# Performance work log

Measured on AMD Instinct MI355X. Metric: run time of the kernel, lower is better.

Reference implementation:

```python
import jax, jax.numpy as jnp
import numpy as np

B, N, IN_DIM, L_DIM, H_DIM, N_CLASSES, FLOW_LEN = 128, 512, 128, 64, 64, 10, 4


def setup_inputs() -> dict:
    key = jax.random.key(0)
    ks = jax.random.split(key, 20)
    s = 0.05
    return {
        "gs": jax.random.uniform(ks[0], (B, N, N), dtype=jnp.float32),
        "hs": jax.random.normal(ks[1], (B, N, IN_DIM), dtype=jnp.float32),
        "labels": jax.random.randint(ks[2], (B,), 0, N_CLASSES),
        "eps": jax.random.normal(ks[3], (B, N, 1), dtype=jnp.float32),
        "W_s": jax.random.normal(ks[4], (IN_DIM, L_DIM), dtype=jnp.float32) * s,
        "b_s": jnp.zeros((L_DIM,), jnp.float32),
        "W_mu": jax.random.normal(ks[5], (L_DIM, 1), dtype=jnp.float32) * s,
        "b_mu": jnp.zeros((1,), jnp.float32),
        "W_lv": jax.random.normal(ks[6], (L_DIM, 1), dtype=jnp.float32) * s,
        "b_lv": jnp.zeros((1,), jnp.float32),
        "W_dec": jax.random.normal(ks[7], (1, L_DIM), dtype=jnp.float32) * s,
        "b_dec": jnp.zeros((L_DIM,), jnp.float32),
        "W1": jax.random.normal(ks[8], (L_DIM, H_DIM), dtype=jnp.float32) * s,
        "b1": jnp.zeros((H_DIM,), jnp.float32),
        "W2": jax.random.normal(ks[9], (H_DIM, N_CLASSES), dtype=jnp.float32) * s,
        "b2": jnp.zeros((N_CLASSES,), jnp.float32),
        "beta": jax.random.uniform(ks[10], (1,), jnp.float32, 0.0, 100.0),
        "fw": jax.random.normal(ks[11], (FLOW_LEN,), dtype=jnp.float32) * 0.1,
        "fb": jax.random.normal(ks[12], (FLOW_LEN,), dtype=jnp.float32) * 0.1,
        "fs": jax.random.normal(ks[13], (FLOW_LEN,), dtype=jnp.float32) * 0.1,
    }


def reference(gs, hs, labels, eps, W_s, b_s, W_mu, b_mu, W_lv, b_lv,
              W_dec, b_dec, W1, b1, W2, b2, beta, fw, fb, fs):
    relu = jax.nn.relu
    # norm_g: g / g.sum(1) (torch broadcast divides column j by row-sum deg[j])
    deg = gs.sum(axis=2)                       # [B, N]
    g = gs / deg[:, None, :]                   # [B, N, N]

    def gcn(g, h, W, b):
        return relu(jnp.einsum('bij,bjf->bif', g, h) @ W + b)

    h = gcn(g, hs, W_s, b_s)                   # [B, N, L]
    r = h
    mu = gcn(g, h, W_mu, b_mu)                 # [B, N, 1]
    logvar = gcn(g, h, W_lv, b_lv)             # [B, N, 1]
    sigma = jnp.exp(0.5 * logvar)
    z0 = eps * sigma + mu                      # reparameterize (training)

    # 4-step planar flow on scalar latent; log-det accumulated on pre-transform z
    z = z0
    log_jac = jnp.zeros_like(z0)
    for k in range(FLOW_LEN):
        t = jnp.tanh(fw[k] * z + fb[k])
        det = 1.0 + fs[k] * fw[k] * (1.0 - t * t)
        log_jac = log_jac + jnp.log(jnp.abs(det) + 1e-7)
        z = z + fs[k] * t
    zk = z

    # KL = log q(z0) - log_jac - log p(zk), loggaussian = -0.5*((z-mu)/s)^2 - log(2.5 s)
    logq = -0.5 * ((z0 - mu) / sigma) ** 2 - jnp.log(2.5 * sigma)
    logp = -0.5 * zk ** 2 - jnp.log(jnp.float32(2.5))
    kl = logq - log_jac - logp                 # [B, N, 1]

    zs = jax.nn.sigmoid(beta * zk)             # [B, N, 1]
    d = gcn(g, zs, W_dec, b_dec)               # [B, N, L]
    hg = jnp.einsum('bnl,bn->bl', h, zs[..., 0])  # h.T @ zk, [B, L]

    # classify
    x = relu(hg @ W1 + b1)
    logits = jax.nn.log_softmax(x @ W2 + b2, axis=1)  # [B, C]

    nll = -jnp.mean(logits[jnp.arange(B), labels])
    mse = jnp.mean((r - d) ** 2)
    loss = nll + mse + kl.mean()
    preds = jnp.argmax(logits, axis=1)
    acc = jnp.mean((preds == labels).astype(jnp.float32))
    return jnp.stack([loss, acc])
```

## Files before the change

kernel.cpp:

```cpp
#include <hip/hip_runtime.h>
#include <hip/hip_bf16.h>

#define BB 128
#define NN 512
#define IND 128
#define LD 64
#define NC 10
#define FL 4
#define ROWS (BB*NN)
#define HALF 256
#define QTR 128

#define OFF_ACC 0
#define OFF_RDEG (OFF_ACC + 8)
#define OFF_VM   (OFF_RDEG + ROWS)
#define OFF_VV   (OFF_VM + ROWS)
#define OFF_ZS   (OFF_VV + ROWS)
#define OFF_ZSS  (OFF_ZS + ROWS)
#define OFF_KLP  (OFF_ZSS + ROWS)
#define OFF_MSEP (OFF_KLP + 512)
#define OFF_XHG  (OFF_MSEP + 512)
#define OFF_H    (OFF_XHG + BB*256)
#define OFF_GSB  (OFF_H + ROWS*32)
#define WS_NEED ((size_t)(OFF_GSB + (size_t)ROWS*256) * 4)

typedef __attribute__((ext_vector_type(8))) short short8v;
typedef __attribute__((ext_vector_type(4))) float f32x4;

__device__ inline float wave_reduce(float v) {
    #pragma unroll
    for (int m = 32; m; m >>= 1) v += __shfl_xor(v, m, 64);
    return v;
}

__device__ inline short f2bf(float f) {
    unsigned u = __float_as_uint(f);
    u += 0x7fff + ((u >> 16) & 1);
    return (short)(u >> 16);
}

__device__ inline float bf2f(short s) {
    return __uint_as_float(((unsigned)(unsigned short)s) << 16);
}

__global__ __launch_bounds__(256) void k_deg(const float* __restrict__ gs,
                                             float* __restrict__ rdeg,
                                             float* __restrict__ accums,
                                             unsigned short* __restrict__ gsb) {
    if (blockIdx.x == 0 && threadIdx.x < 8) accums[threadIdx.x] = 0.f;
    int t = threadIdx.x;
    int row = blockIdx.x * 4 + (t >> 6), lane = t & 63;
    const float4* r4 = (const float4*)(gs + (size_t)row * NN) + lane * 2;
    float4 a = r4[0], b = r4[1];
    float s = a.x + a.y + a.z + a.w + b.x + b.y + b.z + b.w;
    float sr = wave_reduce(s);
    if (lane == 0) rdeg[row] = 1.0f / sr;
    if (gsb) {
        short8v v;
        v[0] = f2bf(a.x); v[1] = f2bf(a.y); v[2] = f2bf(a.z); v[3] = f2bf(a.w);
        v[4] = f2bf(b.x); v[5] = f2bf(b.y); v[6] = f2bf(b.z); v[7] = f2bf(b.w);
        *(short8v*)(gsb + (size_t)row * NN + lane * 8) = v;
    }
}

template<bool BF>
__global__ __launch_bounds__(1024) void k_hwgemm(
    const float* __restrict__ gs, const unsigned short* __restrict__ gsb,
    const float* __restrict__ hs, const float* __restrict__ W_s,
    const float* __restrict__ b_s, const float* __restrict__ W_mu,
    const float* __restrict__ W_lv, const float* __restrict__ rdeg_ws,
    unsigned short* __restrict__ h_ws, float* __restrict__ vm_ws,
    float* __restrict__ vv_ws)
{
    __shared__ unsigned short s_hwT[64 * 512];
    __shared__ unsigned short s_h[HALF * 64];
    __shared__ float s_rdeg[NN];

    const int tid = threadIdx.x, lane = tid & 63, wid = tid >> 6;
    const int b = blockIdx.x >> 1, p = blockIdx.x & 1, rbase = p * HALF;

    if (tid < NN) s_rdeg[tid] = rdeg_ws[(size_t)b * NN + tid];

    unsigned short* sWT = s_h;
    {
        const float4* wp = (const float4*)W_s + tid * 2;
        float4 w0 = wp[0], w1 = wp[1];
        int k = tid >> 3, l0 = (tid & 7) * 8;
        float wv[8] = {w0.x, w0.y, w0.z, w0.w, w1.x, w1.y, w1.z, w1.w};
        #pragma unroll
        for (int e = 0; e < 8; ++e) {
            int l = l0 + e;
            int byte = (l * 256 + k * 2) ^ ((l & 7) << 4);
            *(unsigned short*)((char*)sWT + byte) = (unsigned short)f2bf(wv[e]);
        }
    }
    __syncthreads();

    {
        int n0 = wid * 32, cq = lane & 15, koq = lane >> 4;
        f32x4 accB[2][4] = {};
        #pragma unroll
        for (int kk = 0; kk < 4; ++kk) {
            short8v bf[4];
            #pragma unroll
            for (int lt = 0; lt < 4; ++lt) {
                int l = lt * 16 + cq;
                int byte = (l * 256 + (kk * 32 + koq * 8) * 2) ^ ((l & 7) << 4);
                bf[lt] = *(const short8v*)((char*)sWT + byte);
            }
            #pragma unroll
            for (int nt = 0; nt < 2; ++nt) {
                int row = n0 + nt * 16 + cq;
                const float4* hp = (const float4*)(hs + ((size_t)b * NN + row) * IND
                                                   + kk * 32 + koq * 8);
                float4 h0 = hp[0], h1 = hp[1];
                short8v a;
                a[0] = f2bf(h0.x); a[1] = f2bf(h0.y); a[2] = f2bf(h0.z); a[3] = f2bf(h0.w);
                a[4] = f2bf(h1.x); a[5] = f2bf(h1.y); a[6] = f2bf(h1.z); a[7] = f2bf(h1.w);
                #pragma unroll
                for (int lt = 0; lt < 4; ++lt)
                    accB[nt][lt] = __builtin_amdgcn_mfma_f32_16x16x32_bf16(a, bf[lt], accB[nt][lt], 0, 0, 0);
            }
        }
        __syncthreads();
        int r0 = (lane >> 4) * 4;
        #pragma unroll
        for (int nt = 0; nt < 2; ++nt)
            #pragma unroll
            for (int lt = 0; lt < 4; ++lt)
                #pragma unroll
                for (int q = 0; q < 4; ++q) {
                    int n = n0 + nt * 16 + r0 + q;
                    int l = lt * 16 + cq;
                    int byte = (l * 1024 + n * 2) ^ ((l & 7) << 4);
                    *(unsigned short*)((char*)s_hwT + byte) =
                        (unsigned short)f2bf(accB[nt][lt][q] * s_rdeg[n]);
                }
    }
    __syncthreads();

    {
        int cq = lane & 15, koq = lane >> 4;
        int rowl = wid * 16 + cq, rowg = rbase + rowl;
        const unsigned short* A16 = gsb + ((size_t)b * NN + rowg) * NN + koq * 8;
        const float* A32 = gs + ((size_t)b * NN + rowg) * NN + koq * 8;
        f32x4 accC[4] = {};
        for (int kk = 0; kk < 16; ++kk) {
            short8v bf[4];
            #pragma unroll
            for (int lt = 0; lt < 4; ++lt) {
                int l = lt * 16 + cq;
                int byte = (l * 1024 + (kk * 32 + koq * 8) * 2) ^ ((l & 7) << 4);
                bf[lt] = *(const short8v*)((char*)s_hwT + byte);
            }
            short8v a;
            if constexpr (BF) {
                a = *(const short8v*)(A16 + kk * 32);
            } else {
                const float4* gp = (const float4*)(A32 + kk * 32);
                float4 g0 = gp[0], g1 = gp[1];
                a[0] = f2bf(g0.x); a[1] = f2bf(g0.y); a[2] = f2bf(g0.z); a[3] = f2bf(g0.w);
                a[4] = f2bf(g1.x); a[5] = f2bf(g1.y); a[6] = f2bf(g1.z); a[7] = f2bf(g1.w);
            }
            #pragma unroll
            for (int lt = 0; lt < 4; ++lt)
                accC[lt] = __builtin_amdgcn_mfma_f32_16x16x32_bf16(a, bf[lt], accC[lt], 0, 0, 0);
        }
        int r0 = (lane >> 4) * 4;
        float bsv[4];
        #pragma unroll
        for (int lt = 0; lt < 4; ++lt) bsv[lt] = b_s[lt * 16 + cq];
        #pragma unroll
        for (int lt = 0; lt < 4; ++lt)
            #pragma unroll
            for (int q = 0; q < 4; ++q) {
                int nloc = wid * 16 + r0 + q;
                int l = lt * 16 + cq;
                s_h[nloc * 64 + l] = (unsigned short)f2bf(fmaxf(accC[lt][q] + bsv[lt], 0.f));
            }
    }
    __syncthreads();

    {
        int rowl = tid >> 2, off = (tid & 3) * 16;
        unsigned short* dst = h_ws + ((size_t)(b * NN + rbase + rowl)) * 64 + off;
        const unsigned short* src = &s_h[rowl * 64 + off];
        *(short8v*)dst = *(const short8v*)src;
        *(short8v*)(dst + 8) = *(const short8v*)(src + 8);
    }

    {
        int g16 = tid >> 4, l16 = tid & 15;
        float wmu[4], wlv[4];
        #pragma unroll
        for (int e = 0; e < 4; ++e) { wmu[e] = W_mu[l16 * 4 + e]; wlv[e] = W_lv[l16 * 4 + e]; }
        #pragma unroll
        for (int rr = 0; rr < 4; ++rr) {
            int rowl = g16 * 4 + rr;
            const unsigned short* hp = &s_h[rowl * 64 + l16 * 4];
            float pm = 0.f, pv = 0.f;
            #pragma unroll
            for (int e = 0; e < 4; ++e) {
                float hv = bf2f((short)hp[e]);
                pm += hv * wmu[e]; pv += hv * wlv[e];
            }
            #pragma unroll
            for (int m = 1; m <= 8; m <<= 1) {
                pm += __shfl_xor(pm, m, 64);
                pv += __shfl_xor(pv, m, 64);
            }
            if (l16 == 0) {
                float rd = s_rdeg[rbase + rowl];
                vm_ws[(size_t)b * NN + rbase + rowl] = pm * rd;
                vv_ws[(size_t)b * NN + rbase + rowl] = pv * rd;
            }
        }
    }
}

template<bool BF>
__global__ __launch_bounds__(512) void k_muflow(
    const float* __restrict__ gs, const unsigned short* __restrict__ gsb,
    const float* __restrict__ vm_ws, const float* __restrict__ vv_ws,
    const float* __restrict__ eps, const float* __restrict__ b_mu,
    const float* __restrict__ b_lv, const float* __restrict__ beta,
    const float* __restrict__ fw, const float* __restrict__ fb,
    const float* __restrict__ fs, const float* __restrict__ rdeg_ws,
    float* __restrict__ zs_ws, float* __restrict__ zss_ws,
    float* __restrict__ klp)
{
    __shared__ unsigned short s_bmu[NN], s_blv[NN];
    __shared__ float s_mp[QTR], s_lp[QTR];
    __shared__ float s_fin[8];
    const int tid = threadIdx.x, lane = tid & 63, wid = tid >> 6;
    const int b = blockIdx.x >> 2, qb = blockIdx.x & 3, rbase = qb * QTR;

    if (tid < NN) {
        s_bmu[tid] = (unsigned short)f2bf(vm_ws[(size_t)b * NN + tid]);
        s_blv[tid] = (unsigned short)f2bf(vv_ws[(size_t)b * NN + tid]);
    }
    __syncthreads();

    const int cq = lane & 15, koq = lane >> 4;
    const int rowl = wid * 16 + cq, rowg = rbase + rowl;
    const unsigned short* A16 = gsb + ((size_t)b * NN + rowg) * NN + koq * 8;
    const float* A32 = gs + ((size_t)b * NN + rowg) * NN + koq * 8;
    const char* bptr = (cq == 1) ? (const char*)s_blv : (const char*)s_bmu;
    f32x4 acc = {0.f, 0.f, 0.f, 0.f};
    const short8v bz = {0, 0, 0, 0, 0, 0, 0, 0};
    #pragma unroll 4
    for (int kk = 0; kk < 16; ++kk) {
        short8v a;
        if constexpr (BF) {
            a = *(const short8v*)(A16 + kk * 32);
        } else {
            const float4* gp = (const float4*)(A32 + kk * 32);
            float4 g0 = gp[0], g1 = gp[1];
            a[0] = f2bf(g0.x); a[1] = f2bf(g0.y); a[2] = f2bf(g0.z); a[3] = f2bf(g0.w);
            a[4] = f2bf(g1.x); a[5] = f2bf(g1.y); a[6] = f2bf(g1.z); a[7] = f2bf(g1.w);
        }
        short8v bl = *(const short8v*)(bptr + (kk * 32 + koq * 8) * 2);
        short8v bfrag = (cq < 2) ? bl : bz;
        acc = __builtin_amdgcn_mfma_f32_16x16x32_bf16(a, bfrag, acc, 0, 0, 0);
    }
    int r0 = (lane >> 4) * 4;
    if (cq == 0) {
        #pragma unroll
        for (int q2 = 0; q2 < 4; ++q2) s_mp[wid * 16 + r0 + q2] = acc[q2];
    } else if (cq == 1) {
        #pragma unroll
        for (int q2 = 0; q2 < 4; ++q2) s_lp[wid * 16 + r0 + q2] = acc[q2];
    }
    __syncthreads();

    float my_kl = 0.f;
    if (tid < QTR) {
        int rg = rbase + tid;
        float mu = fmaxf(s_mp[tid] + b_mu[0], 0.f);
        float lv = fmaxf(s_lp[tid] + b_lv[0], 0.f);
        float sigma = expf(0.5f * lv);
        float z0 = eps[(size_t)b * NN + rg] * sigma + mu;
        float z = z0, lj = 0.f;
        #pragma unroll
        for (int k = 0; k < FL; ++k) {
            float tt = tanhf(fw[k] * z + fb[k]);
            float det = 1.f + fs[k] * fw[k] * (1.f - tt * tt);
            lj += logf(fabsf(det) + 1e-7f);
            z += fs[k] * tt;
        }
        float e0 = (z0 - mu) / sigma;
        float logq = -0.5f * e0 * e0 - logf(2.5f * sigma);
        float logp = -0.5f * z * z - logf(2.5f);
        my_kl = logq - lj - logp;
        float zv = 1.f / (1.f + expf(-beta[0] * z));
        float rd = rdeg_ws[(size_t)b * NN + rg];
        zs_ws[(size_t)b * NN + rg] = zv;
        zss_ws[(size_t)b * NN + rg] = zv * rd;
    }
    float kv = wave_reduce(my_kl);
    if (lane == 0) s_fin[wid] = kv;
    __syncthreads();
    if (tid == 0) {
        float ks = 0.f;
        #pragma unroll
        for (int w = 0; w < 8; ++w) ks += s_fin[w];
        klp[blockIdx.x] = ks;
    }
}

template<bool BF>
__global__ __launch_bounds__(512) void k_dec(
    const float* __restrict__ gs, const unsigned short* __restrict__ gsb,
    const float* __restrict__ zss_ws, const float* __restrict__ zs_ws,
    const unsigned short* __restrict__ h_ws, const float* __restrict__ W_dec,
    const float* __restrict__ b_dec, float* __restrict__ msep,
    float* __restrict__ xhg)
{
    __shared__ unsigned short s_bz[NN];
    __shared__ float s_zs[QTR];
    __shared__ float s_dp[QTR];
    __shared__ float s_red[8 * 68];
    __shared__ float s_fin[8];
    const int tid = threadIdx.x, lane = tid & 63, wid = tid >> 6;
    const int b = blockIdx.x >> 2, qb = blockIdx.x & 3, rbase = qb * QTR;

    if (tid < NN) s_bz[tid] = (unsigned short)f2bf(zss_ws[(size_t)b * NN + tid]);
    if (tid < QTR) s_zs[tid] = zs_ws[(size_t)b * NN + rbase + tid];
    __syncthreads();

    const int cq = lane & 15, koq = lane >> 4;
    const int rowl = wid * 16 + cq, rowg = rbase + rowl;
    const unsigned short* A16 = gsb + ((size_t)b * NN + rowg) * NN + koq * 8;
    const float* A32 = gs + ((size_t)b * NN + rowg) * NN + koq * 8;
    f32x4 acc = {0.f, 0.f, 0.f, 0.f};
    const short8v bz = {0, 0, 0, 0, 0, 0, 0, 0};
    #pragma unroll 4
    for (int kk = 0; kk < 16; ++kk) {
        short8v a;
        if constexpr (BF) {
            a = *(const short8v*)(A16 + kk * 32);
        } else {
            const float4* gp = (const float4*)(A32 + kk * 32);
            float4 g0 = gp[0], g1 = gp[1];
            a[0] = f2bf(g0.x); a[1] = f2bf(g0.y); a[2] = f2bf(g0.z); a[3] = f2bf(g0.w);
            a[4] = f2bf(g1.x); a[5] = f2bf(g1.y); a[6] = f2bf(g1.z); a[7] = f2bf(g1.w);
        }
        short8v bl = *(const short8v*)((const char*)s_bz + (kk * 32 + koq * 8) * 2);
        short8v bfrag = (cq == 0) ? bl : bz;
        acc = __builtin_amdgcn_mfma_f32_16x16x32_bf16(a, bfrag, acc, 0, 0, 0);
    }
    int r0 = (lane >> 4) * 4;
    if (cq == 0) {
        #pragma unroll
        for (int q2 = 0; q2 < 4; ++q2) s_dp[wid * 16 + r0 + q2] = acc[q2];
    }
    __syncthreads();

    float wd = W_dec[lane], bd = b_dec[lane];
    float msacc = 0.f, hgacc = 0.f;
    #pragma unroll 4
    for (int r = 0; r < 16; ++r) {
        int rl = wid * 16 + r, rg = rbase + rl;
        float dval = fmaxf(s_dp[rl] * wd + bd, 0.f);
        float hval = bf2f((short)h_ws[((size_t)b * NN + rg) * 64 + lane]);
        float diff = hval - dval;
        msacc += diff * diff;
        hgacc += hval * s_zs[rl];
    }
    s_red[wid * 68 + lane] = hgacc;
    float mv = wave_reduce(msacc);
    if (lane == 0) s_fin[wid] = mv;
    __syncthreads();
    if (tid == 0) {
        float ms = 0.f;
        #pragma unroll
        for (int w = 0; w < 8; ++w) ms += s_fin[w];
        msep[blockIdx.x] = ms;
    }
    if (wid == 0) {
        float hgv = 0.f;
        #pragma unroll
        for (int w = 0; w < 8; ++w) hgv += s_red[w * 68 + lane];
        xhg[(size_t)b * 256 + qb * 64 + lane] = hgv;
    }
}

__global__ __launch_bounds__(64) void k_cls(const float* __restrict__ xhg,
                                            const float* __restrict__ klp,
                                            const float* __restrict__ msep,
                                            const float* __restrict__ W1,
                                            const float* __restrict__ b1,
                                            const float* __restrict__ W2,
                                            const float* __restrict__ b2,
                                            const int* __restrict__ labels,
                                            float* __restrict__ accums,
                                            float* __restrict__ out)
{
    __shared__ float s_hg[64], s_x[64], s_lg[12];
    int b = blockIdx.x, l = threadIdx.x;
    s_hg[l] = xhg[(size_t)b * 256 + l] + xhg[(size_t)b * 256 + 64 + l]
            + xhg[(size_t)b * 256 + 128 + l] + xhg[(size_t)b * 256 + 192 + l];
    if (l == 0) atomicAdd(&accums[0], klp[4*b] + klp[4*b+1] + klp[4*b+2] + klp[4*b+3]);
    if (l == 1) atomicAdd(&accums[1], msep[4*b] + msep[4*b+1] + msep[4*b+2] + msep[4*b+3]);
    __syncthreads();
    float x = b1[l];
    #pragma unroll 8
    for (int k = 0; k < LD; ++k) x += s_hg[k] * W1[k * LD + l];
    s_x[l] = fmaxf(x, 0.f);
    __syncthreads();
    if (l < NC) {
        float lg = b2[l];
        #pragma unroll 8
        for (int k = 0; k < LD; ++k) lg += s_x[k] * W2[k * NC + l];
        s_lg[l] = lg;
    }
    __syncthreads();
    if (l == 0) {
        float mx = s_lg[0]; int pred = 0;
        #pragma unroll
        for (int c = 1; c < NC; ++c) if (s_lg[c] > mx) { mx = s_lg[c]; pred = c; }
        float se = 0.f;
        #pragma unroll
        for (int c = 0; c < NC; ++c) se += expf(s_lg[c] - mx);
        int lab = labels[b];
        atomicAdd(&accums[2], -(s_lg[lab] - (mx + logf(se))));
        if (pred == lab) atomicAdd(&accums[3], 1.0f);
        __threadfence();
        unsigned old = atomicAdd((unsigned*)&accums[4], 1u);
        if (old == BB - 1) {
            float kk = atomicAdd(&accums[0], 0.f);
            float mm = atomicAdd(&accums[1], 0.f);
            float nn = atomicAdd(&accums[2], 0.f);
            float aa = atomicAdd(&accums[3], 0.f);
            out[0] = nn / (float)BB
                   + mm / ((float)BB * NN * LD)
                   + kk / ((float)BB * NN);
            out[1] = aa / (float)BB;
        }
    }
}

extern "C" void kernel_launch(void* const* d_in, const int* in_sizes, int n_in,
                              void* d_out, int out_size, void* d_ws, size_t ws_size,
                              hipStream_t stream) {
    const float* gs    = (const float*)d_in[0];
    const float* hs    = (const float*)d_in[1];
    const int*   labels= (const int*)d_in[2];
    const float* eps   = (const float*)d_in[3];
    const float* W_s   = (const float*)d_in[4];
    const float* b_s   = (const float*)d_in[5];
    const float* W_mu  = (const float*)d_in[6];
    const float* b_mu  = (const float*)d_in[7];
    const float* W_lv  = (const float*)d_in[8];
    const float* b_lv  = (const float*)d_in[9];
    const float* W_dec = (const float*)d_in[10];
    const float* b_dec = (const float*)d_in[11];
    const float* W1    = (const float*)d_in[12];
    const float* b1    = (const float*)d_in[13];
    const float* W2    = (const float*)d_in[14];
    const float* b2    = (const float*)d_in[15];
    const float* beta  = (const float*)d_in[16];
    const float* fw    = (const float*)d_in[17];
    const float* fb    = (const float*)d_in[18];
    const float* fs    = (const float*)d_in[19];

    float* ws      = (float*)d_ws;
    float* accums  = ws + OFF_ACC;
    float* rdeg    = ws + OFF_RDEG;
    float* vm_ws   = ws + OFF_VM;
    float* vv_ws   = ws + OFF_VV;
    float* zs_ws   = ws + OFF_ZS;
    float* zss_ws  = ws + OFF_ZSS;
    float* klp     = ws + OFF_KLP;
    float* msep    = ws + OFF_MSEP;
    float* xhg     = ws + OFF_XHG;
    unsigned short* h_ws = (unsigned short*)(ws + OFF_H);
    unsigned short* gsb  = (unsigned short*)(ws + OFF_GSB);
    float* out = (float*)d_out;

    bool big = ws_size >= WS_NEED;

    k_deg<<<ROWS / 4, 256, 0, stream>>>(gs, rdeg, accums, big ? gsb : nullptr);
    if (big) {
        k_hwgemm<true><<<2 * BB, 1024, 0, stream>>>(gs, gsb, hs, W_s, b_s, W_mu, W_lv,
                                                    rdeg, h_ws, vm_ws, vv_ws);
        k_muflow<true><<<4 * BB, 512, 0, stream>>>(gs, gsb, vm_ws, vv_ws, eps, b_mu, b_lv,
                                                   beta, fw, fb, fs, rdeg, zs_ws, zss_ws,
                                                   klp);
        k_dec<true><<<4 * BB, 512, 0, stream>>>(gs, gsb, zss_ws, zs_ws, h_ws, W_dec, b_dec,
                                                msep, xhg);
    } else {
        k_hwgemm<false><<<2 * BB, 1024, 0, stream>>>(gs, gsb, hs, W_s, b_s, W_mu, W_lv,
                                                     rdeg, h_ws, vm_ws, vv_ws);
        k_muflow<false><<<4 * BB, 512, 0, stream>>>(gs, gsb, vm_ws, vv_ws, eps, b_mu, b_lv,
                                                    beta, fw, fb, fs, rdeg, zs_ws, zss_ws,
                                                    klp);
        k_dec<false><<<4 * BB, 512, 0, stream>>>(gs, gsb, zss_ws, zs_ws, h_ws, W_dec, b_dec,
                                                 msep, xhg);
    }
    k_cls<<<BB, 64, 0, stream>>>(xhg, klp, msep, W1, b1, W2, b2, labels, accums, out);
}
```

Measured before the change: 101.9 us.

## Split hs@W_s into separate kernel, quarter-row GEMM blocks, fuse classifier into decoder

Moves the per-graph hs@W_s product out of the fused GEMM kernel into its own FP32 kernel that writes a transposed bf16 hwT buffer. This lets the aggregation GEMM run on 512 blocks of 512 threads instead of 256 blocks of 1024, which improves CU occupancy. The h@W_mu and h@W_lv projections move into the GEMM epilogue, and the classifier kernel is folded into k_dec using a per-graph last-block-wins counter. The cost is an extra launch and an hwT round-trip through global memory, plus atomic accumulation of xhg and the MSE partial sums. k_deg now zeroes these accumulators.

```diff
diff --git a/kernel.cpp b/kernel.cpp
--- a/kernel.cpp
+++ b/kernel.cpp
@@ -8,19 +8,20 @@
 #define NC 10
 #define FL 4
 #define ROWS (BB*NN)
-#define HALF 256
 #define QTR 128
 
 #define OFF_ACC 0
-#define OFF_RDEG (OFF_ACC + 8)
+#define OFF_PCNT 8
+#define OFF_MSES 136
+#define OFF_RDEG 264
 #define OFF_VM   (OFF_RDEG + ROWS)
 #define OFF_VV   (OFF_VM + ROWS)
 #define OFF_ZS   (OFF_VV + ROWS)
 #define OFF_ZSS  (OFF_ZS + ROWS)
 #define OFF_KLP  (OFF_ZSS + ROWS)
-#define OFF_MSEP (OFF_KLP + 512)
-#define OFF_XHG  (OFF_MSEP + 512)
-#define OFF_H    (OFF_XHG + BB*256)
+#define OFF_XHG  (OFF_KLP + 512)
+#define OFF_HWT  (OFF_XHG + BB*64)
+#define OFF_H    (OFF_HWT + ROWS*32)
 #define OFF_GSB  (OFF_H + ROWS*32)
 #define WS_NEED ((size_t)(OFF_GSB + (size_t)ROWS*256) * 4)
 
@@ -43,13 +44,18 @@
     return __uint_as_float(((unsigned)(unsigned short)s) << 16);
 }
 
-__global__ __launch_bounds__(256) void k_deg(const float* __restrict__ gs,
-                                             float* __restrict__ rdeg,
-                                             float* __restrict__ accums,
+__global__ __launch_bounds__(512) void k_deg(const float* __restrict__ gs,
+                                             float* __restrict__ ws_f,
                                              unsigned short* __restrict__ gsb) {
-    if (blockIdx.x == 0 && threadIdx.x < 8) accums[threadIdx.x] = 0.f;
     int t = threadIdx.x;
-    int row = blockIdx.x * 4 + (t >> 6), lane = t & 63;
+    if (blockIdx.x == 0) {
+        for (int i = t; i < 264; i += 512) ws_f[i] = 0.f;
+    }
+    if (blockIdx.x >= 1 && blockIdx.x <= 16) {
+        ws_f[OFF_XHG + (blockIdx.x - 1) * 512 + t] = 0.f;
+    }
+    float* rdeg = ws_f + OFF_RDEG;
+    int row = blockIdx.x * 8 + (t >> 6), lane = t & 63;
     const float4* r4 = (const float4*)(gs + (size_t)row * NN) + lane * 2;
     float4 a = r4[0], b = r4[1];
     float s = a.x + a.y + a.z + a.w + b.x + b.y + b.z + b.w;
@@ -63,157 +69,128 @@
     }
 }
 
+__global__ __launch_bounds__(256) void k_hw(const float* __restrict__ hs,
+                                            const float* __restrict__ W_s,
+                                            const float* __restrict__ rdeg,
+                                            unsigned short* __restrict__ hwT) {
+    __shared__ float sW[IND * LD];
+    __shared__ float shs[16 * 132];
+    __shared__ unsigned short sT[64][24];
+    int t = threadIdx.x;
+    for (int i = t; i < IND * LD; i += 256) sW[i] = W_s[i];
+    int row0 = blockIdx.x * 16;
+    for (int i = t; i < 16 * IND; i += 256)
+        shs[(i >> 7) * 132 + (i & 127)] = hs[(size_t)row0 * IND + i];
+    __syncthreads();
+    int l = t & 63, rg = t >> 6;
+    float acc[4] = {0.f, 0.f, 0.f, 0.f};
+    for (int f = 0; f < IND; ++f) {
+        float w = sW[f * LD + l];
+        #pragma unroll
+        for (int r = 0; r < 4; ++r)
+            acc[r] += shs[(rg * 4 + r) * 132 + f] * w;
+    }
+    #pragma unroll
+    for (int r = 0; r < 4; ++r) {
+        int row = row0 + rg * 4 + r;
+        sT[l][rg * 4 + r] = (unsigned short)f2bf(acc[r] * rdeg[row]);
+    }
+    __syncthreads();
+    if (t < 64) {
+        int b = row0 >> 9, n0 = row0 & 511;
+        unsigned short* dst = hwT + ((size_t)b * 64 + t) * 512 + n0;
+        short8v v0, v1;
+        #pragma unroll
+        for (int e = 0; e < 8; ++e) { v0[e] = (short)sT[t][e]; v1[e] = (short)sT[t][8 + e]; }
+        *(short8v*)dst = v0;
+        *(short8v*)(dst + 8) = v1;
+    }
+}
+
 template<bool BF>
-__global__ __launch_bounds__(1024) void k_hwgemm(
+__global__ __launch_bounds__(512) void k_gemm(
     const float* __restrict__ gs, const unsigned short* __restrict__ gsb,
-    const float* __restrict__ hs, const float* __restrict__ W_s,
-    const float* __restrict__ b_s, const float* __restrict__ W_mu,
-    const float* __restrict__ W_lv, const float* __restrict__ rdeg_ws,
-    unsigned short* __restrict__ h_ws, float* __restrict__ vm_ws,
-    float* __restrict__ vv_ws)
+    const unsigned short* __restrict__ hwT, const float* __restrict__ b_s,
+    const float* __restrict__ W_mu, const float* __restrict__ W_lv,
+    const float* __restrict__ rdeg_ws, unsigned short* __restrict__ h_ws,
+    float* __restrict__ vm_ws, float* __restrict__ vv_ws)
 {
     __shared__ unsigned short s_hwT[64 * 512];
-    __shared__ unsigned short s_h[HALF * 64];
-    __shared__ float s_rdeg[NN];
-
+    __shared__ float s_rdeg[QTR];
     const int tid = threadIdx.x, lane = tid & 63, wid = tid >> 6;
-    const int b = blockIdx.x >> 1, p = blockIdx.x & 1, rbase = p * HALF;
-
-    if (tid < NN) s_rdeg[tid] = rdeg_ws[(size_t)b * NN + tid];
-
-    unsigned short* sWT = s_h;
+    const int b = blockIdx.x >> 2, qb = blockIdx.x & 3, rbase = qb * QTR;
+
     {
-        const float4* wp = (const float4*)W_s + tid * 2;
-        float4 w0 = wp[0], w1 = wp[1];
-        int k = tid >> 3, l0 = (tid & 7) * 8;
-        float wv[8] = {w0.x, w0.y, w0.z, w0.w, w1.x, w1.y, w1.z, w1.w};
-        #pragma unroll
-        for (int e = 0; e < 8; ++e) {
-            int l = l0 + e;
-            int byte = (l * 256 + k * 2) ^ ((l & 7) << 4);
-            *(unsigned short*)((char*)sWT + byte) = (unsigned short)f2bf(wv[e]);
-        }
-    }
-    __syncthreads();
-
-    {
-        int n0 = wid * 32, cq = lane & 15, koq = lane >> 4;
-        f32x4 accB[2][4] = {};
-        #pragma unroll
-        for (int kk = 0; kk < 4; ++kk) {
-            short8v bf[4];
-            #pragma unroll
-            for (int lt = 0; lt < 4; ++lt) {
-                int l = lt * 16 + cq;
-                int byte = (l * 256 + (kk * 32 + koq * 8) * 2) ^ ((l & 7) << 4);
-                bf[lt] = *(const short8v*)((char*)sWT + byte);
-            }
-            #pragma unroll
-            for (int nt = 0; nt < 2; ++nt) {
-                int row = n0 + nt * 16 + cq;
-                const float4* hp = (const float4*)(hs + ((size_t)b * NN + row) * IND
-                                                   + kk * 32 + koq * 8);
-                float4 h0 = hp[0], h1 = hp[1];
-                short8v a;
-                a[0] = f2bf(h0.x); a[1] = f2bf(h0.y); a[2] = f2bf(h0.z); a[3] = f2bf(h0.w);
-                a[4] = f2bf(h1.x); a[5] = f2bf(h1.y); a[6] = f2bf(h1.z); a[7] = f2bf(h1.w);
-                #pragma unroll
-                for (int lt = 0; lt < 4; ++lt)
-                    accB[nt][lt] = __builtin_amdgcn_mfma_f32_16x16x32_bf16(a, bf[lt], accB[nt][lt], 0, 0, 0);
-            }
-        }
-        __syncthreads();
-        int r0 = (lane >> 4) * 4;
-        #pragma unroll
-        for (int nt = 0; nt < 2; ++nt)
-            #pragma unroll
-            for (int lt = 0; lt < 4; ++lt)
-                #pragma unroll
-                for (int q = 0; q < 4; ++q) {
-                    int n = n0 + nt * 16 + r0 + q;
-                    int l = lt * 16 + cq;
-                    int byte = (l * 1024 + n * 2) ^ ((l & 7) << 4);
-                    *(unsigned short*)((char*)s_hwT + byte) =
-                        (unsigned short)f2bf(accB[nt][lt][q] * s_rdeg[n]);
-                }
-    }
-    __syncthreads();
-
-    {
-        int cq = lane & 15, koq = lane >> 4;
-        int rowl = wid * 16 + cq, rowg = rbase + rowl;
-        const unsigned short* A16 = gsb + ((size_t)b * NN + rowg) * NN + koq * 8;
-        const float* A32 = gs + ((size_t)b * NN + rowg) * NN + koq * 8;
-        f32x4 accC[4] = {};
-        for (int kk = 0; kk < 16; ++kk) {
-            short8v bf[4];
-            #pragma unroll
-            for (int lt = 0; lt < 4; ++lt) {
-                int l = lt * 16 + cq;
-                int byte = (l * 1024 + (kk * 32 + koq * 8) * 2) ^ ((l & 7) << 4);
-                bf[lt] = *(const short8v*)((char*)s_hwT + byte);
-            }
-            short8v a;
-            if constexpr (BF) {
-                a = *(const short8v*)(A16 + kk * 32);
-            } else {
-                const float4* gp = (const float4*)(A32 + kk * 32);
-                float4 g0 = gp[0], g1 = gp[1];
-                a[0] = f2bf(g0.x); a[1] = f2bf(g0.y); a[2] = f2bf(g0.z); a[3] = f2bf(g0.w);
-                a[4] = f2bf(g1.x); a[5] = f2bf(g1.y); a[6] = f2bf(g1.z); a[7] = f2bf(g1.w);
-            }
-            #pragma unroll
-            for (int lt = 0; lt < 4; ++lt)
-                accC[lt] = __builtin_amdgcn_mfma_f32_16x16x32_bf16(a, bf[lt], accC[lt], 0, 0, 0);
-        }
-        int r0 = (lane >> 4) * 4;
-        float bsv[4];
-        #pragma unroll
-        for (int lt = 0; lt < 4; ++lt) bsv[lt] = b_s[lt * 16 + cq];
-        #pragma unroll
-        for (int lt = 0; lt < 4; ++lt)
-            #pragma unroll
-            for (int q = 0; q < 4; ++q) {
-                int nloc = wid * 16 + r0 + q;
-                int l = lt * 16 + cq;
-                s_h[nloc * 64 + l] = (unsigned short)f2bf(fmaxf(accC[lt][q] + bsv[lt], 0.f));
-            }
-    }
-    __syncthreads();
-
-    {
-        int rowl = tid >> 2, off = (tid & 3) * 16;
-        unsigned short* dst = h_ws + ((size_t)(b * NN + rbase + rowl)) * 64 + off;
-        const unsigned short* src = &s_h[rowl * 64 + off];
-        *(short8v*)dst = *(const short8v*)src;
-        *(short8v*)(dst + 8) = *(const short8v*)(src + 8);
-    }
-
-    {
-        int g16 = tid >> 4, l16 = tid & 15;
-        float wmu[4], wlv[4];
-        #pragma unroll
-        for (int e = 0; e < 4; ++e) { wmu[e] = W_mu[l16 * 4 + e]; wlv[e] = W_lv[l16 * 4 + e]; }
-        #pragma unroll
-        for (int rr = 0; rr < 4; ++rr) {
-            int rowl = g16 * 4 + rr;
-            const unsigned short* hp = &s_h[rowl * 64 + l16 * 4];
-            float pm = 0.f, pv = 0.f;
-            #pragma unroll
-            for (int e = 0; e < 4; ++e) {
-                float hv = bf2f((short)hp[e]);
-                pm += hv * wmu[e]; pv += hv * wlv[e];
-            }
-            #pragma unroll
-            for (int m = 1; m <= 8; m <<= 1) {
-                pm += __shfl_xor(pm, m, 64);
-                pv += __shfl_xor(pv, m, 64);
-            }
-            if (l16 == 0) {
-                float rd = s_rdeg[rbase + rowl];
-                vm_ws[(size_t)b * NN + rbase + rowl] = pm * rd;
-                vv_ws[(size_t)b * NN + rbase + rowl] = pv * rd;
-            }
+        const unsigned short* src = hwT + (size_t)b * 64 * 512;
+        #pragma unroll
+        for (int v = 0; v < 8; ++v) {
+            int flat = tid * 64 + v * 8;
+            int l = flat >> 9, n = flat & 511;
+            short8v d = *(const short8v*)(src + flat);
+            *(short8v*)((char*)s_hwT + ((l * 1024 + n * 2) ^ ((l & 7) << 4))) = d;
+        }
+    }
+    if (tid < QTR) s_rdeg[tid] = rdeg_ws[(size_t)b * NN + rbase + tid];
+    __syncthreads();
+
+    const int cq = lane & 15, koq = lane >> 4;
+    const int rowg = rbase + wid * 16 + cq;
+    const unsigned short* A16 = gsb + ((size_t)b * NN + rowg) * NN + koq * 8;
+    const float* A32 = gs + ((size_t)b * NN + rowg) * NN + koq * 8;
+    f32x4 acc0 = {0.f,0.f,0.f,0.f}, acc1 = acc0, acc2 = acc0, acc3 = acc0;
+    #pragma unroll 4
+    for (int kk = 0; kk < 16; ++kk) {
+        short8v bf0, bf1, bf2, bf3;
+        {
+            int kb = (kk * 32 + koq * 8) * 2;
+            bf0 = *(const short8v*)((char*)s_hwT + ((( 0 + cq) * 1024 + kb) ^ ((( 0 + cq) & 7) << 4)));
+            bf1 = *(const short8v*)((char*)s_hwT + (((16 + cq) * 1024 + kb) ^ (((16 + cq) & 7) << 4)));
+            bf2 = *(const short8v*)((char*)s_hwT + (((32 + cq) * 1024 + kb) ^ (((32 + cq) & 7) << 4)));
+            bf3 = *(const short8v*)((char*)s_hwT + (((48 + cq) * 1024 + kb) ^ (((48 + cq) & 7) << 4)));
+        }
+        short8v a;
+        if constexpr (BF) {
+            a = *(const short8v*)(A16 + kk * 32);
+        } else {
+            const float4* gp = (const float4*)(A32 + kk * 32);
+            float4 g0 = gp[0], g1 = gp[1];
+            a[0] = f2bf(g0.x); a[1] = f2bf(g0.y); a[2] = f2bf(g0.z); a[3] = f2bf(g0.w);
+            a[4] = f2bf(g1.x); a[5] = f2bf(g1.y); a[6] = f2bf(g1.z); a[7] = f2bf(g1.w);
+        }
+        acc0 = __builtin_amdgcn_mfma_f32_16x16x32_bf16(a, bf0, acc0, 0, 0, 0);
+        acc1 = __builtin_amdgcn_mfma_f32_16x16x32_bf16(a, bf1, acc1, 0, 0, 0);
+        acc2 = __builtin_amdgcn_mfma_f32_16x16x32_bf16(a, bf2, acc2, 0, 0, 0);
+        acc3 = __builtin_amdgcn_mfma_f32_16x16x32_bf16(a, bf3, acc3, 0, 0, 0);
+    }
+
+    const int r0 = koq * 4;
+    float bs0 = b_s[cq], bs1 = b_s[16 + cq], bs2 = b_s[32 + cq], bs3 = b_s[48 + cq];
+    float wm0 = W_mu[cq], wm1 = W_mu[16 + cq], wm2 = W_mu[32 + cq], wm3 = W_mu[48 + cq];
+    float wv0 = W_lv[cq], wv1 = W_lv[16 + cq], wv2 = W_lv[32 + cq], wv3 = W_lv[48 + cq];
+    #pragma unroll
+    for (int q = 0; q < 4; ++q) {
+        int rowl = wid * 16 + r0 + q;
+        int rg = rbase + rowl;
+        float h0 = fmaxf(acc0[q] + bs0, 0.f);
+        float h1 = fmaxf(acc1[q] + bs1, 0.f);
+        float h2 = fmaxf(acc2[q] + bs2, 0.f);
+        float h3 = fmaxf(acc3[q] + bs3, 0.f);
+        unsigned short* hb = h_ws + ((size_t)b * NN + rg) * 64;
+        hb[ 0 + cq] = (unsigned short)f2bf(h0);
+        hb[16 + cq] = (unsigned short)f2bf(h1);
+        hb[32 + cq] = (unsigned short)f2bf(h2);
+        hb[48 + cq] = (unsigned short)f2bf(h3);
+        float pm = h0 * wm0 + h1 * wm1 + h2 * wm2 + h3 * wm3;
+        float pv = h0 * wv0 + h1 * wv1 + h2 * wv2 + h3 * wv3;
+        #pragma unroll
+        for (int mk = 8; mk; mk >>= 1) {
+            pm += __shfl_xor(pm, mk, 64);
+            pv += __shfl_xor(pv, mk, 64);
+        }
+        if (cq == 0) {
+            float rd = s_rdeg[rowl];
+            vm_ws[(size_t)b * NN + rg] = pm * rd;
+            vv_ws[(size_t)b * NN + rg] = pv * rd;
         }
     }
 }
@@ -242,7 +219,7 @@
     __syncthreads();
 
     const int cq = lane & 15, koq = lane >> 4;
-    const int rowl = wid * 16 + cq, rowg = rbase + rowl;
+    const int rowg = rbase + wid * 16 + cq;
     const unsigned short* A16 = gsb + ((size_t)b * NN + rowg) * NN + koq * 8;
     const float* A32 = gs + ((size_t)b * NN + rowg) * NN + koq * 8;
     const char* bptr = (cq == 1) ? (const char*)s_blv : (const char*)s_bmu;
@@ -313,23 +290,33 @@
     const float* __restrict__ gs, const unsigned short* __restrict__ gsb,
     const float* __restrict__ zss_ws, const float* __restrict__ zs_ws,
     const unsigned short* __restrict__ h_ws, const float* __restrict__ W_dec,
-    const float* __restrict__ b_dec, float* __restrict__ msep,
-    float* __restrict__ xhg)
+    const float* __restrict__ b_dec, const float* __restrict__ klp,
+    const float* __restrict__ W1, const float* __restrict__ b1,
+    const float* __restrict__ W2, const float* __restrict__ b2,
+    const int* __restrict__ labels, float* __restrict__ ws_f,
+    float* __restrict__ out)
 {
     __shared__ unsigned short s_bz[NN];
     __shared__ float s_zs[QTR];
     __shared__ float s_dp[QTR];
     __shared__ float s_red[8 * 68];
     __shared__ float s_fin[8];
+    __shared__ float s_hg[64], s_x[64], s_lg[12];
+    __shared__ int s_win;
     const int tid = threadIdx.x, lane = tid & 63, wid = tid >> 6;
     const int b = blockIdx.x >> 2, qb = blockIdx.x & 3, rbase = qb * QTR;
 
+    float* accums = ws_f + OFF_ACC;
+    unsigned* pcnt = (unsigned*)(ws_f + OFF_PCNT);
+    float* mses = ws_f + OFF_MSES;
+    float* xhg = ws_f + OFF_XHG;
+
     if (tid < NN) s_bz[tid] = (unsigned short)f2bf(zss_ws[(size_t)b * NN + tid]);
     if (tid < QTR) s_zs[tid] = zs_ws[(size_t)b * NN + rbase + tid];
     __syncthreads();
 
     const int cq = lane & 15, koq = lane >> 4;
-    const int rowl = wid * 16 + cq, rowg = rbase + rowl;
+    const int rowg = rbase + wid * 16 + cq;
     const unsigned short* A16 = gsb + ((size_t)b * NN + rowg) * NN + koq * 8;
     const float* A32 = gs + ((size_t)b * NN + rowg) * NN + koq * 8;
     f32x4 acc = {0.f, 0.f, 0.f, 0.f};
@@ -375,67 +362,58 @@
         float ms = 0.f;
         #pragma unroll
         for (int w = 0; w < 8; ++w) ms += s_fin[w];
-        msep[blockIdx.x] = ms;
+        atomicAdd(&mses[b], ms);
     }
     if (wid == 0) {
         float hgv = 0.f;
         #pragma unroll
         for (int w = 0; w < 8; ++w) hgv += s_red[w * 68 + lane];
-        xhg[(size_t)b * 256 + qb * 64 + lane] = hgv;
-    }
-}
-
-__global__ __launch_bounds__(64) void k_cls(const float* __restrict__ xhg,
-                                            const float* __restrict__ klp,
-                                            const float* __restrict__ msep,
-                                            const float* __restrict__ W1,
-                                            const float* __restrict__ b1,
-                                            const float* __restrict__ W2,
-                                            const float* __restrict__ b2,
-                                            const int* __restrict__ labels,
-                                            float* __restrict__ accums,
-                                            float* __restrict__ out)
-{
-    __shared__ float s_hg[64], s_x[64], s_lg[12];
-    int b = blockIdx.x, l = threadIdx.x;
-    s_hg[l] = xhg[(size_t)b * 256 + l] + xhg[(size_t)b * 256 + 64 + l]
-            + xhg[(size_t)b * 256 + 128 + l] + xhg[(size_t)b * 256 + 192 + l];
-    if (l == 0) atomicAdd(&accums[0], klp[4*b] + klp[4*b+1] + klp[4*b+2] + klp[4*b+3]);
-    if (l == 1) atomicAdd(&accums[1], msep[4*b] + msep[4*b+1] + msep[4*b+2] + msep[4*b+3]);
-    __syncthreads();
-    float x = b1[l];
-    #pragma unroll 8
-    for (int k = 0; k < LD; ++k) x += s_hg[k] * W1[k * LD + l];
-    s_x[l] = fmaxf(x, 0.f);
-    __syncthreads();
-    if (l < NC) {
-        float lg = b2[l];
+        atomicAdd(&xhg[(size_t)b * 64 + lane], hgv);
+    }
+    __syncthreads();
+    if (tid == 0) s_win = (atomicAdd(&pcnt[b], 1u) == 3u) ? 1 : 0;
+    __syncthreads();
+
+    if (s_win && wid == 0) {
+        float hg = atomicAdd(&xhg[(size_t)b * 64 + lane], 0.f);
+        s_hg[lane] = hg;
+        float x = b1[lane];
         #pragma unroll 8
-        for (int k = 0; k < LD; ++k) lg += s_x[k] * W2[k * NC + l];
-        s_lg[l] = lg;
-    }
-    __syncthreads();
-    if (l == 0) {
-        float mx = s_lg[0]; int pred = 0;
-        #pragma unroll
-        for (int c = 1; c < NC; ++c) if (s_lg[c] > mx) { mx = s_lg[c]; pred = c; }
-        float se = 0.f;
-        #pragma unroll
-        for (int c = 0; c < NC; ++c) se += expf(s_lg[c] - mx);
-        int lab = labels[b];
-        atomicAdd(&accums[2], -(s_lg[lab] - (mx + logf(se))));
-        if (pred == lab) atomicAdd(&accums[3], 1.0f);
-        __threadfence();
-        unsigned old = atomicAdd((unsigned*)&accums[4], 1u);
-        if (old == BB - 1) {
-            float kk = atomicAdd(&accums[0], 0.f);
-            float mm = atomicAdd(&accums[1], 0.f);
-            float nn = atomicAdd(&accums[2], 0.f);
-            float aa = atomicAdd(&accums[3], 0.f);
-            out[0] = nn / (float)BB
-                   + mm / ((float)BB * NN * LD)
-                   + kk / ((float)BB * NN);
-            out[1] = aa / (float)BB;
+        for (int k = 0; k < LD; ++k) x += s_hg[k] * W1[k * LD + lane];
+        s_x[lane] = fmaxf(x, 0.f);
+        if (lane < NC) {
+            float lg = b2[lane];
+            #pragma unroll 8
+            for (int k = 0; k < LD; ++k) lg += s_x[k] * W2[k * NC + lane];
+            s_lg[lane] = lg;
+        }
+        if (lane == 0) {
+            float mx = s_lg[0]; int pred = 0;
+            #pragma unroll
+            for (int c = 1; c < NC; ++c) if (s_lg[c] > mx) { mx = s_lg[c]; pred = c; }
+            float se = 0.f;
+            #pragma unroll
+            for (int c = 0; c < NC; ++c) se += expf(s_lg[c] - mx);
+            int lab = labels[b];
+            float nll = -(s_lg[lab] - (mx + logf(se)));
+            float kl4 = klp[4*b] + klp[4*b+1] + klp[4*b+2] + klp[4*b+3];
+            float msS = atomicAdd(&mses[b], 0.f);
+            atomicAdd(&accums[0], kl4);
+            atomicAdd(&accums[1], msS);
+            atomicAdd(&accums[2], nll);
+            if (pred == lab) atomicAdd(&accums[3], 1.0f);
+            __threadfence();
+            unsigned old = atomicAdd((unsigned*)&accums[4], 1u);
+            if (old == BB - 1) {
+                float kk = atomicAdd(&accums[0], 0.f);
+                float mm = atomicAdd(&accums[1], 0.f);
+                float nn = atomicAdd(&accums[2], 0.f);
+                float aa = atomicAdd(&accums[3], 0.f);
+                out[0] = nn / (float)BB
+                       + mm / ((float)BB * NN * LD)
+                       + kk / ((float)BB * NN);
+                out[1] = aa / (float)BB;
+            }
         }
     }
 }
@@ -465,38 +443,36 @@
     const float* fs    = (const float*)d_in[19];
 
     float* ws      = (float*)d_ws;
-    float* accums  = ws + OFF_ACC;
     float* rdeg    = ws + OFF_RDEG;
     float* vm_ws   = ws + OFF_VM;
     float* vv_ws   = ws + OFF_VV;
     float* zs_ws   = ws + OFF_ZS;
     float* zss_ws  = ws + OFF_ZSS;
     float* klp     = ws + OFF_KLP;
-    float* msep    = ws + OFF_MSEP;
-    float* xhg     = ws + OFF_XHG;
+    unsigned short* hwT  = (unsigned short*)(ws + OFF_HWT);
     unsigned short* h_ws = (unsigned short*)(ws + OFF_H);
     unsigned short* gsb  = (unsigned short*)(ws + OFF_GSB);
     float* out = (float*)d_out;
 
     bool big = ws_size >= WS_NEED;
 
-    k_deg<<<ROWS / 4, 256, 0, stream>>>(gs, rdeg, accums, big ? gsb : nullptr);
+    k_deg<<<ROWS / 8, 512, 0, stream>>>(gs, ws, big ? gsb : nullptr);
+    k_hw<<<ROWS / 16, 256, 0, stream>>>(hs, W_s, rdeg, hwT);
     if (big) {
-        k_hwgemm<true><<<2 * BB, 1024, 0, stream>>>(gs, gsb, hs, W_s, b_s, W_mu, W_lv,
-                                                    rdeg, h_ws, vm_ws, vv_ws);
+        k_gemm<true><<<4 * BB, 512, 0, stream>>>(gs, gsb, hwT, b_s, W_mu, W_lv,
+                                                 rdeg, h_ws, vm_ws, vv_ws);
         k_muflow<true><<<4 * BB, 512, 0, stream>>>(gs, gsb, vm_ws, vv_ws, eps, b_mu, b_lv,
                                                    beta, fw, fb, fs, rdeg, zs_ws, zss_ws,
                                                    klp);
         k_dec<true><<<4 * BB, 512, 0, stream>>>(gs, gsb, zss_ws, zs_ws, h_ws, W_dec, b_dec,
-                                                msep, xhg);
+                                                klp, W1, b1, W2, b2, labels, ws, out);
     } else {
-        k_hwgemm<false><<<2 * BB, 1024, 0, stream>>>(gs, gsb, hs, W_s, b_s, W_mu, W_lv,
-                                                     rdeg, h_ws, vm_ws, vv_ws);
+        k_gemm<false><<<4 * BB, 512, 0, stream>>>(gs, gsb, hwT, b_s, W_mu, W_lv,
+                                                  rdeg, h_ws, vm_ws, vv_ws);
         k_muflow<false><<<4 * BB, 512, 0, stream>>>(gs, gsb, vm_ws, vv_ws, eps, b_mu, b_lv,
                                                     beta, fw, fb, fs, rdeg, zs_ws, zss_ws,
                                                     klp);
         k_dec<false><<<4 * BB, 512, 0, stream>>>(gs, gsb, zss_ws, zs_ws, h_ws, W_dec, b_dec,
-                                                 msep, xhg);
-    }
-    k_cls<<<BB, 64, 0, stream>>>(xhg, klp, msep, W1, b1, W2, b2, labels, accums, out);
-}
+                                                 klp, W1, b1, W2, b2, labels, ws, out);
+    }
+}
```

New measurement: 131.1 us. +28.7%, slower.
